# Kernel tuning notes

Measured on AMD Instinct MI355X. Metric: run time of the kernel, lower is better.

The kernel has to match this reference:

```python
import jax, jax.numpy as jnp
import numpy as np

NEG_INF = -1e30

def _pool_unpool(x, k):
    # x: [B, C, H, W]. Non-overlapping max pool with window k (floor-mode,
    # matching torch MaxPool2d default), then MaxUnpool: scatter the pooled max
    # back to its argmax location within each window, zeros elsewhere.
    B, C, H, W = x.shape
    Hc, Wc = (H // k) * k, (W // k) * k  # cropped region covered by windows
    xc = x[:, :, :Hc, :Wc]
    # reshape into windows: [B, C, H/k, k, W/k, k] -> [B, C, H/k, W/k, k*k]
    xw = xc.reshape(B, C, Hc // k, k, Wc // k, k).transpose(0, 1, 2, 4, 3, 5)
    xw = xw.reshape(B, C, Hc // k, Wc // k, k * k)
    mx = jnp.max(xw, axis=-1, keepdims=True)
    am = jnp.argmax(xw, axis=-1)  # first max index, matches torch tie-breaking
    onehot = (jnp.arange(k * k) == am[..., None])
    yw = jnp.where(onehot, mx, jnp.zeros_like(mx))
    yc = yw.reshape(B, C, Hc // k, Wc // k, k, k).transpose(0, 1, 2, 4, 3, 5)
    yc = yc.reshape(B, C, Hc, Wc)
    # output_size=size in torch unpool -> pad uncovered border with zeros
    return jnp.pad(yc, ((0, 0), (0, 0), (0, H - Hc), (0, W - Wc)))

def setup_inputs() -> dict:
    key = jax.random.key(0)
    x = jax.random.uniform(key, (16, 1, 1080, 1920), dtype=jnp.float32)
    return {"x": x}

def reference(x):
    k = 3
    x = _pool_unpool(x, k)
    x = _pool_unpool(x, k + 2)
    x = _pool_unpool(x, k + 3)
    return x
```

## Files before the change

### kernel.cpp

```cpp
#include <hip/hip_runtime.h>


#define IMG_H 1080
#define IMG_W 1920
#define TILE_H 30
#define TILE_W 240
#define NT 256

__global__ __launch_bounds__(NT) void pooling_nms_kernel(
    const float* __restrict__ x, float* __restrict__ out) {
    __shared__ float sval[800];
    __shared__ int   spos[800];
    __shared__ float w5val[288];
    __shared__ int   w5pos[288];

    const int t = threadIdx.x;
    const size_t base = (size_t)blockIdx.z * ((size_t)IMG_H * IMG_W) +
                        (size_t)blockIdx.y * TILE_H * IMG_W +
                        (size_t)blockIdx.x * TILE_W;
    const float* src = x + base;
    float* dst = out + base;

    for (int w = t; w < 800; w += NT) {
        const int wr = w / 80;
        const int wc = w - wr * 80;
        const int r0 = wr * 3, c0 = wc * 3;
        float mx = -1.0f;
        int am = 0;
#pragma unroll
        for (int r = 0; r < 3; ++r) {
            const float* p = src + (size_t)(r0 + r) * IMG_W + c0;
            const float v0 = p[0], v1 = p[1], v2 = p[2];
            if (v0 > mx) { mx = v0; am = ((r0 + r) << 8) | c0; }
            if (v1 > mx) { mx = v1; am = ((r0 + r) << 8) | (c0 + 1); }
            if (v2 > mx) { mx = v2; am = ((r0 + r) << 8) | (c0 + 2); }
        }
        sval[w] = mx;
        spos[w] = am;
    }

    for (int i = t; i < (TILE_H * TILE_W / 4); i += NT) {
        const int r = i / (TILE_W / 4);
        const int c4 = i - r * (TILE_W / 4);
        *reinterpret_cast<float4*>(dst + (size_t)r * IMG_W + c4 * 4) =
            make_float4(0.f, 0.f, 0.f, 0.f);
    }
    __syncthreads();

    for (int w = t; w < 288; w += NT) {
        const int a = w / 48;
        const int b = w - a * 48;
        const int rlo = (5 * a) / 3, rhi = (5 * a + 4) / 3;
        const int clo = (5 * b) / 3, chi = (5 * b + 4) / 3;
        float bv = -1.0f;
        int bp = 0x7FFFFFFF;
        for (int r3 = rlo; r3 <= rhi; ++r3)
            for (int c3 = clo; c3 <= chi; ++c3) {
                const int idx = r3 * 80 + c3;
                const float v = sval[idx];
                const int p = spos[idx];
                const int r = p >> 8, c = p & 255;
                const bool in =
                    ((unsigned)(r - 5 * a) < 5u) & ((unsigned)(c - 5 * b) < 5u);
                if (in && (v > bv || (v == bv && p < bp))) { bv = v; bp = p; }
            }
        w5val[w] = bv;
        w5pos[w] = bp;
    }
    __syncthreads();

    for (int w = t; w < 200; w += NT) {
        const int a = w / 40;
        const int b = w - a * 40;
        const int rlo = (6 * a) / 5;
        const int clo = (6 * b) / 5;
        float bv = -1.0f;
        int bp = 0x7FFFFFFF;
#pragma unroll
        for (int dr = 0; dr < 2; ++dr)
#pragma unroll
            for (int dc = 0; dc < 2; ++dc) {
                const int idx = (rlo + dr) * 48 + (clo + dc);
                const float v = w5val[idx];
                const int p = w5pos[idx];
                const int r = p >> 8, c = p & 255;
                const bool in = (v >= 0.0f) &
                                ((unsigned)(r - 6 * a) < 6u) &
                                ((unsigned)(c - 6 * b) < 6u);
                if (in && (v > bv || (v == bv && p < bp))) { bv = v; bp = p; }
            }
        if (bv >= 0.0f) {
            const int r = bp >> 8, c = bp & 255;
            dst[(size_t)r * IMG_W + c] = bv;
        }
    }
}

extern "C" void kernel_launch(void* const* d_in, const int* in_sizes, int n_in,
                              void* d_out, int out_size, void* d_ws, size_t ws_size,
                              hipStream_t stream) {
    const float* x = (const float*)d_in[0];
    float* out = (float*)d_out;
    dim3 grid(IMG_W / TILE_W, IMG_H / TILE_H, 16);
    pooling_nms_kernel<<<grid, NT, 0, stream>>>(x, out);
}
```

Baseline: 255.0 us.

## Assemble each 30x30 output tile in LDS and write it out once per wavefront

Splits the work so each 64-lane wavefront owns one 30x30 tile (the LCM of the window sizes), with four tiles per block, instead of a block covering a 30x240 strip. The output tile is zeroed and filled in shared memory, then written to global memory with float2 stores. This replaces the separate global zero pass and the scattered single-float writes of the maxima. The new layout leaves many lanes idle in the later stages, and the 120-byte row pitch limits stores to float2 width.

```diff
diff --git a/kernel.cpp b/kernel.cpp
--- a/kernel.cpp
+++ b/kernel.cpp
@@ -3,96 +3,101 @@
 
 #define IMG_H 1080
 #define IMG_W 1920
-#define TILE_H 30
-#define TILE_W 240
 #define NT 256
 
 __global__ __launch_bounds__(NT) void pooling_nms_kernel(
     const float* __restrict__ x, float* __restrict__ out) {
-    __shared__ float sval[800];
-    __shared__ int   spos[800];
-    __shared__ float w5val[288];
-    __shared__ int   w5pos[288];
+    __shared__ float comp[4][900];
+    __shared__ float sv[4][100];
+    __shared__ int   sp[4][100];
+    __shared__ float w5v[4][36];
+    __shared__ int   w5p[4][36];
 
     const int t = threadIdx.x;
+    const int w = t >> 6;
+    const int ln = t & 63;
+
+    const int stc = blockIdx.x * 4 + w;
+    const int str = blockIdx.y;
     const size_t base = (size_t)blockIdx.z * ((size_t)IMG_H * IMG_W) +
-                        (size_t)blockIdx.y * TILE_H * IMG_W +
-                        (size_t)blockIdx.x * TILE_W;
+                        (size_t)str * 30 * IMG_W + (size_t)stc * 30;
     const float* src = x + base;
     float* dst = out + base;
 
-    for (int w = t; w < 800; w += NT) {
-        const int wr = w / 80;
-        const int wc = w - wr * 80;
-        const int r0 = wr * 3, c0 = wc * 3;
-        float mx = -1.0f;
-        int am = 0;
+    float4* c4 = reinterpret_cast<float4*>(comp[w]);
+    for (int i = ln; i < 225; i += 64) c4[i] = make_float4(0.f, 0.f, 0.f, 0.f);
+
 #pragma unroll
-        for (int r = 0; r < 3; ++r) {
-            const float* p = src + (size_t)(r0 + r) * IMG_W + c0;
-            const float v0 = p[0], v1 = p[1], v2 = p[2];
-            if (v0 > mx) { mx = v0; am = ((r0 + r) << 8) | c0; }
-            if (v1 > mx) { mx = v1; am = ((r0 + r) << 8) | (c0 + 1); }
-            if (v2 > mx) { mx = v2; am = ((r0 + r) << 8) | (c0 + 2); }
+    for (int b = 0; b < 2; ++b) {
+        const int win = b * 64 + ln;
+        if (win < 100) {
+            const int wr = win / 10, wc = win - wr * 10;
+            const float* p = src + (size_t)(wr * 3) * IMG_W + wc * 3;
+            float mx = -1.0f;
+            int am = 0;
+#pragma unroll
+            for (int r = 0; r < 3; ++r) {
+                const float v0 = p[(size_t)r * IMG_W + 0];
+                const float v1 = p[(size_t)r * IMG_W + 1];
+                const float v2 = p[(size_t)r * IMG_W + 2];
+                const int rr = wr * 3 + r, cc = wc * 3;
+                if (v0 > mx) { mx = v0; am = (rr << 5) | cc; }
+                if (v1 > mx) { mx = v1; am = (rr << 5) | (cc + 1); }
+                if (v2 > mx) { mx = v2; am = (rr << 5) | (cc + 2); }
+            }
+            sv[w][win] = mx;
+            sp[w][win] = am;
         }
-        sval[w] = mx;
-        spos[w] = am;
-    }
-
-    for (int i = t; i < (TILE_H * TILE_W / 4); i += NT) {
-        const int r = i / (TILE_W / 4);
-        const int c4 = i - r * (TILE_W / 4);
-        *reinterpret_cast<float4*>(dst + (size_t)r * IMG_W + c4 * 4) =
-            make_float4(0.f, 0.f, 0.f, 0.f);
     }
     __syncthreads();
 
-    for (int w = t; w < 288; w += NT) {
-        const int a = w / 48;
-        const int b = w - a * 48;
+    if (ln < 36) {
+        const int a = ln / 6, b = ln - (ln / 6) * 6;
         const int rlo = (5 * a) / 3, rhi = (5 * a + 4) / 3;
         const int clo = (5 * b) / 3, chi = (5 * b + 4) / 3;
         float bv = -1.0f;
         int bp = 0x7FFFFFFF;
         for (int r3 = rlo; r3 <= rhi; ++r3)
             for (int c3 = clo; c3 <= chi; ++c3) {
-                const int idx = r3 * 80 + c3;
-                const float v = sval[idx];
-                const int p = spos[idx];
-                const int r = p >> 8, c = p & 255;
+                const int idx = r3 * 10 + c3;
+                const float v = sv[w][idx];
+                const int p = sp[w][idx];
+                const int r = p >> 5, c = p & 31;
                 const bool in =
                     ((unsigned)(r - 5 * a) < 5u) & ((unsigned)(c - 5 * b) < 5u);
                 if (in && (v > bv || (v == bv && p < bp))) { bv = v; bp = p; }
             }
-        w5val[w] = bv;
-        w5pos[w] = bp;
+        w5v[w][ln] = bv;
+        w5p[w][ln] = bp;
     }
     __syncthreads();
 
-    for (int w = t; w < 200; w += NT) {
-        const int a = w / 40;
-        const int b = w - a * 40;
-        const int rlo = (6 * a) / 5;
-        const int clo = (6 * b) / 5;
+    if (ln < 25) {
+        const int a = ln / 5, b = ln - (ln / 5) * 5;
+        const int rlo = (6 * a) / 5, clo = (6 * b) / 5;
         float bv = -1.0f;
         int bp = 0x7FFFFFFF;
 #pragma unroll
         for (int dr = 0; dr < 2; ++dr)
 #pragma unroll
             for (int dc = 0; dc < 2; ++dc) {
-                const int idx = (rlo + dr) * 48 + (clo + dc);
-                const float v = w5val[idx];
-                const int p = w5pos[idx];
-                const int r = p >> 8, c = p & 255;
+                const int idx = (rlo + dr) * 6 + (clo + dc);
+                const float v = w5v[w][idx];
+                const int p = w5p[w][idx];
+                const int r = p >> 5, c = p & 31;
                 const bool in = (v >= 0.0f) &
                                 ((unsigned)(r - 6 * a) < 6u) &
                                 ((unsigned)(c - 6 * b) < 6u);
                 if (in && (v > bv || (v == bv && p < bp))) { bv = v; bp = p; }
             }
-        if (bv >= 0.0f) {
-            const int r = bp >> 8, c = bp & 255;
-            dst[(size_t)r * IMG_W + c] = bv;
-        }
+        if (bv >= 0.0f) comp[w][(bp >> 5) * 30 + (bp & 31)] = bv;
+    }
+    __syncthreads();
+
+    const float2* c2 = reinterpret_cast<const float2*>(comp[w]);
+    for (int i = ln; i < 450; i += 64) {
+        const int r = i / 15, cc = i - r * 15;
+        *reinterpret_cast<float2*>(dst + (size_t)r * IMG_W + cc * 2) = c2[i];
     }
 }
 
@@ -101,6 +106,6 @@
                               hipStream_t stream) {
     const float* x = (const float*)d_in[0];
     float* out = (float*)d_out;
-    dim3 grid(IMG_W / TILE_W, IMG_H / TILE_H, 16);
+    dim3 grid(IMG_W / 120, IMG_H / 30, 16);
     pooling_nms_kernel<<<grid, NT, 0, stream>>>(x, out);
 }
```

New measurement: 249.5 us. 2.1% less time.
